# Performance work log

Measured on AMD Instinct MI355X. Metric: run time of the kernel, lower is better.

## Reference

```python
import jax, jax.numpy as jnp
import numpy as np


def setup_inputs() -> dict:
    key = jax.random.key(0)
    k1, k2, k3, k4 = jax.random.split(key, 4)
    B, C, H, W = 8, 512, 64, 64  # h must equal w per the broadcast in the original
    opt = jax.random.normal(k1, (B, C, H, W), dtype=jnp.float32)
    sar = jax.random.normal(k2, (B, C, H, W), dtype=jnp.float32)
    # 1x1 conv weights, shape [out_c, in_c] (kernel spatial dims are 1x1)
    W_opt = jax.random.normal(k3, (C, C), dtype=jnp.float32) * (2.0 / C) ** 0.5
    W_sar = jax.random.normal(k4, (C, C), dtype=jnp.float32) * (2.0 / C) ** 0.5
    return {"opt": opt, "sar": sar, "W_opt": W_opt, "W_sar": W_sar}


def _branch(x, Wc):
    # 1x1 conv: per-pixel channel mixing. Q = K = V (same conv applied to same input).
    f = jnp.einsum('oc,bchw->bohw', Wc, x)            # (b,c,h,w)
    # S[b,c,i,j] = sum_h Q[b,c,h,i] * K[b,c,h,j]  (transpose(2,3) @ original)
    S = jnp.einsum('bchi,bchj->bcij', f, f)           # (b,c,w,w)
    # nn.Softmax() with no dim on 4D -> softmax over channel dim (axis=1)
    S = jax.nn.softmax(S, axis=1)
    return f, S


def reference(opt, sar, W_opt, W_sar):
    V_opt, S_opt = _branch(opt, W_opt)
    V_sar, S_sar = _branch(sar, W_sar)
    hadamard = S_opt * S_sar                          # (b,c,w,w); h==w lets it broadcast with V
    Att = (V_opt * hadamard) * (V_sar * hadamard)
    return Att
```

## Files before the change

kernel.cpp:

```cpp
#include <hip/hip_runtime.h>
#include <cstdint>

#define CCH 512
#define HW  4096
#define WDIM 64
#define NBATCH 8
#define CHW ((size_t)CCH * HW)

typedef __attribute__((ext_vector_type(8))) short bf16x8;
typedef __attribute__((ext_vector_type(4))) float f32x4;

__device__ __forceinline__ unsigned short f2bf(float x) {
  unsigned u = __float_as_uint(x);
  unsigned r = (u + 0x7FFFu + ((u >> 16) & 1u)) >> 16;
  return (unsigned short)r;
}
__device__ __forceinline__ float bf2f(unsigned short h) {
  return __uint_as_float(((unsigned)h) << 16);
}

__device__ __forceinline__ void gl_lds16(const void* g, void* l) {
  __builtin_amdgcn_global_load_lds(
      (const __attribute__((address_space(1))) void*)g,
      (__attribute__((address_space(3))) void*)l, 16, 0, 0);
}

__global__ __launch_bounds__(256) void wsplit_k(
    const float* __restrict__ Wo, const float* __restrict__ Wsr,
    unsigned short* __restrict__ Whl) {
  const int br = blockIdx.y;
  const float* W = br ? Wsr : Wo;
  const int i = blockIdx.x * 256 + threadIdx.x;
  const float x = W[i];
  const unsigned short h = f2bf(x);
  unsigned short* dst = Whl + (size_t)br * 524288;
  dst[i] = h;
  dst[262144 + i] = f2bf(x - bf2f(h));
}

__global__ __launch_bounds__(256) void splitT_k(
    const float* __restrict__ opt, const float* __restrict__ sar,
    unsigned short* __restrict__ Xth, unsigned short* __restrict__ Xtl,
    int b0) {
  const int z = blockIdx.z;
  const int br = z & 1, bl = z >> 1;
  const float* X = (br ? sar : opt) + (size_t)(b0 + bl) * CHW;
  unsigned short* oh = Xth + (size_t)z * CHW;
  unsigned short* ol = Xtl + (size_t)z * CHW;
  const int p0 = blockIdx.x * 64, c0 = blockIdx.y * 64;

  __shared__ float ts[64][65];
  const int tid = threadIdx.x;

  const int pl = (tid & 15) * 4;
#pragma unroll
  for (int rr = 0; rr < 4; ++rr) {
    const int cl = rr * 16 + (tid >> 4);
    float4 v = *(const float4*)&X[(size_t)(c0 + cl) * HW + p0 + pl];
    ts[cl][pl + 0] = v.x;
    ts[cl][pl + 1] = v.y;
    ts[cl][pl + 2] = v.z;
    ts[cl][pl + 3] = v.w;
  }
  __syncthreads();

  const int prow = tid >> 2;
  const int cch = (tid & 3) * 16;
  unsigned short hb[16], lb[16];
#pragma unroll
  for (int k = 0; k < 16; ++k) {
    const float x = ts[cch + k][prow];
    const unsigned short h = f2bf(x);
    hb[k] = h;
    lb[k] = f2bf(x - bf2f(h));
  }
  const size_t ob = (size_t)(p0 + prow) * CCH + c0 + cch;
  *(uint4*)&oh[ob] = *(uint4*)&hb[0];
  *(uint4*)&oh[ob + 8] = *(uint4*)&hb[8];
  *(uint4*)&ol[ob] = *(uint4*)&lb[0];
  *(uint4*)&ol[ob + 8] = *(uint4*)&lb[8];
}

__global__ __launch_bounds__(256, 4) void mfma_conv_k(
    const unsigned short* __restrict__ Whl,
    const unsigned short* __restrict__ Xth,
    const unsigned short* __restrict__ Xtl,
    float* __restrict__ F) {
  const int z = blockIdx.z;
  const int br = z & 1;
  const unsigned short* Ah_g = Whl + (size_t)br * 524288;
  const unsigned short* Al_g = Ah_g + 262144;
  const unsigned short* Bh_g = Xth + (size_t)z * CHW;
  const unsigned short* Bl_g = Xtl + (size_t)z * CHW;
  const int n0 = blockIdx.x * 128, m0 = blockIdx.y * 128;

  __shared__ unsigned short Ahs[128 * 32];
  __shared__ unsigned short Als[128 * 32];
  __shared__ unsigned short Bhs[128 * 32];
  __shared__ unsigned short Bls[128 * 32];

  const int tid = threadIdx.x;
  const int wave = tid >> 6, lane = tid & 63;
  const int wm = (wave >> 1) * 64, wn = (wave & 1) * 64;

  f32x4 acc[4][4] = {};

  const int rl = lane >> 2;
  const int kc = (((lane & 3) ^ ((lane >> 3) & 3)) * 8);

  for (int k0 = 0; k0 < CCH; k0 += 32) {
    __syncthreads();
#pragma unroll
    for (int q = 0; q < 2; ++q) {
      const int rbase = wave * 32 + q * 16;
      const int r = rbase + rl;
      gl_lds16(Ah_g + (size_t)(m0 + r) * CCH + k0 + kc, &Ahs[rbase * 32]);
      gl_lds16(Al_g + (size_t)(m0 + r) * CCH + k0 + kc, &Als[rbase * 32]);
      gl_lds16(Bh_g + (size_t)(n0 + r) * CCH + k0 + kc, &Bhs[rbase * 32]);
      gl_lds16(Bl_g + (size_t)(n0 + r) * CCH + k0 + kc, &Bls[rbase * 32]);
    }
    __syncthreads();

    const int fr = lane & 15;
    const int kh = (((lane >> 4) ^ ((lane >> 1) & 3)) * 8);
    bf16x8 ah[4], al[4], bh[4], bl[4];
#pragma unroll
    for (int i = 0; i < 4; ++i) {
      ah[i] = *(const bf16x8*)&Ahs[(wm + i * 16 + fr) * 32 + kh];
      al[i] = *(const bf16x8*)&Als[(wm + i * 16 + fr) * 32 + kh];
      bh[i] = *(const bf16x8*)&Bhs[(wn + i * 16 + fr) * 32 + kh];
      bl[i] = *(const bf16x8*)&Bls[(wn + i * 16 + fr) * 32 + kh];
    }
#pragma unroll
    for (int i = 0; i < 4; ++i)
#pragma unroll
      for (int j = 0; j < 4; ++j) {
        acc[i][j] = __builtin_amdgcn_mfma_f32_16x16x32_bf16(ah[i], bh[j], acc[i][j], 0, 0, 0);
        acc[i][j] = __builtin_amdgcn_mfma_f32_16x16x32_bf16(ah[i], bl[j], acc[i][j], 0, 0, 0);
        acc[i][j] = __builtin_amdgcn_mfma_f32_16x16x32_bf16(al[i], bh[j], acc[i][j], 0, 0, 0);
      }
  }

  float* Fb = F + (size_t)z * CHW;
  const int col = lane & 15, rq = (lane >> 4) * 4;
#pragma unroll
  for (int i = 0; i < 4; ++i)
#pragma unroll
    for (int j = 0; j < 4; ++j) {
      const int n = n0 + wn + j * 16 + col;
#pragma unroll
      for (int r = 0; r < 4; ++r) {
        const int m = m0 + wm + i * 16 + rq + r;
        Fb[(size_t)m * HW + n] = acc[i][j][r];
      }
    }
}

#define FT_S 72
__global__ __launch_bounds__(256, 4) void gram_k(
    const float* __restrict__ F, float* __restrict__ S) {
  const size_t base = ((size_t)blockIdx.y * CCH + blockIdx.x) * HW;
  const float* Fc = F + base;
  float* Sc = S + base;

  __shared__ float Fs[64][68];
  __shared__ unsigned short FtH[64 * FT_S];
  __shared__ unsigned short FtL[64 * FT_S];

  const int tid = threadIdx.x;

  {
    const int h = tid >> 2;
    const int w0 = (tid & 3) * 16;
    const float* src = &Fc[h * 64 + w0];
    float4 v0 = *(const float4*)(src + 0);
    float4 v1 = *(const float4*)(src + 4);
    float4 v2 = *(const float4*)(src + 8);
    float4 v3 = *(const float4*)(src + 12);
    *(float4*)&Fs[h][w0 + 0]  = v0;
    *(float4*)&Fs[h][w0 + 4]  = v1;
    *(float4*)&Fs[h][w0 + 8]  = v2;
    *(float4*)&Fs[h][w0 + 12] = v3;
  }
  __syncthreads();

  {
    const int w = tid & 63;
    const int hc = (tid >> 6) * 16;
    unsigned short hb[16], lb[16];
#pragma unroll
    for (int k = 0; k < 16; ++k) {
      const float x = Fs[hc + k][w];
      const unsigned short h = f2bf(x);
      hb[k] = h;
      lb[k] = f2bf(x - bf2f(h));
    }
    unsigned short* dh = &FtH[w * FT_S + hc];
    unsigned short* dl = &FtL[w * FT_S + hc];
    *(uint4*)(dh + 0) = *(uint4*)&hb[0];
    *(uint4*)(dh + 8) = *(uint4*)&hb[8];
    *(uint4*)(dl + 0) = *(uint4*)&lb[0];
    *(uint4*)(dl + 8) = *(uint4*)&lb[8];
  }
  __syncthreads();

  const int wave = tid >> 6, lane = tid & 63;
  const int wm = (wave >> 1) * 32, wn = (wave & 1) * 32;
  const int fr = lane & 15, kq = (lane >> 4) * 8;

  f32x4 acc[2][2] = {};
#pragma unroll
  for (int kcc = 0; kcc < 2; ++kcc) {
    bf16x8 ah[2], al[2], bh[2], bl[2];
#pragma unroll
    for (int i = 0; i < 2; ++i) {
      ah[i] = *(const bf16x8*)&FtH[(wm + i * 16 + fr) * FT_S + kcc * 32 + kq];
      al[i] = *(const bf16x8*)&FtL[(wm + i * 16 + fr) * FT_S + kcc * 32 + kq];
      bh[i] = *(const bf16x8*)&FtH[(wn + i * 16 + fr) * FT_S + kcc * 32 + kq];
      bl[i] = *(const bf16x8*)&FtL[(wn + i * 16 + fr) * FT_S + kcc * 32 + kq];
    }
#pragma unroll
    for (int i = 0; i < 2; ++i)
#pragma unroll
      for (int j = 0; j < 2; ++j) {
        acc[i][j] = __builtin_amdgcn_mfma_f32_16x16x32_bf16(ah[i], bh[j], acc[i][j], 0, 0, 0);
        acc[i][j] = __builtin_amdgcn_mfma_f32_16x16x32_bf16(ah[i], bl[j], acc[i][j], 0, 0, 0);
        acc[i][j] = __builtin_amdgcn_mfma_f32_16x16x32_bf16(al[i], bh[j], acc[i][j], 0, 0, 0);
      }
  }

  const int rq = (lane >> 4) * 4;
#pragma unroll
  for (int i = 0; i < 2; ++i)
#pragma unroll
    for (int j = 0; j < 2; ++j) {
      const int n = wn + j * 16 + fr;
#pragma unroll
      for (int r = 0; r < 4; ++r) {
        const int m = wm + i * 16 + rq + r;
        Sc[m * 64 + n] = acc[i][j][r];
      }
    }
}

__global__ __launch_bounds__(1024, 8) void softmax_fuse_k(
    const float* __restrict__ S, const float* __restrict__ Fbuf,
    float* __restrict__ Out) {
  const int i = blockIdx.x;
  const int b = blockIdx.y;
  const int tid = threadIdx.x;
  const int jl = (tid & 15) * 4;
  const int g = tid >> 4;

  const size_t rowO = (size_t)(b * 2) * CHW + (size_t)i * WDIM;
  const size_t rowS = rowO + CHW;

  float mo[4], lo[4], ms[4], ls[4];
#pragma unroll
  for (int k = 0; k < 4; ++k) { mo[k] = -1e30f; lo[k] = 0.f; ms[k] = -1e30f; ls[k] = 0.f; }

#pragma unroll
  for (int cc = 0; cc < 8; ++cc) {
    const int c = g * 8 + cc;
    const size_t off = (size_t)c * HW + jl;
    float4 xo = *(const float4*)&S[rowO + off];
    float4 xs = *(const float4*)&S[rowS + off];
    float xov[4] = {xo.x, xo.y, xo.z, xo.w};
    float xsv[4] = {xs.x, xs.y, xs.z, xs.w};
#pragma unroll
    for (int k = 0; k < 4; ++k) {
      float nm = fmaxf(mo[k], xov[k]);
      lo[k] = lo[k] * __expf(mo[k] - nm) + __expf(xov[k] - nm);
      mo[k] = nm;
      nm = fmaxf(ms[k], xsv[k]);
      ls[k] = ls[k] * __expf(ms[k] - nm) + __expf(xsv[k] - nm);
      ms[k] = nm;
    }
  }

  __shared__ float sm[2][64][64];
  __shared__ float sl[2][64][64];
  __shared__ float Mf[2][64];
  __shared__ float Li[2][64];

  *(float4*)&sm[0][g][jl] = make_float4(mo[0], mo[1], mo[2], mo[3]);
  *(float4*)&sl[0][g][jl] = make_float4(lo[0], lo[1], lo[2], lo[3]);
  *(float4*)&sm[1][g][jl] = make_float4(ms[0], ms[1], ms[2], ms[3]);
  *(float4*)&sl[1][g][jl] = make_float4(ls[0], ls[1], ls[2], ls[3]);
  __syncthreads();

  if (tid < 128) {
    const int br = tid >> 6, j = tid & 63;
    float M = -1e30f;
#pragma unroll 16
    for (int t = 0; t < 64; ++t) M = fmaxf(M, sm[br][t][j]);
    float L = 0.f;
#pragma unroll 16
    for (int t = 0; t < 64; ++t) L += sl[br][t][j] * __expf(sm[br][t][j] - M);
    Mf[br][j] = M;
    Li[br][j] = 1.f / L;
  }
  __syncthreads();

  float4 Mo4 = *(const float4*)&Mf[0][jl];
  float4 iLo4 = *(const float4*)&Li[0][jl];
  float4 Ms4 = *(const float4*)&Mf[1][jl];
  float4 iLs4 = *(const float4*)&Li[1][jl];
  float Mov[4] = {Mo4.x, Mo4.y, Mo4.z, Mo4.w};
  float iLov[4] = {iLo4.x, iLo4.y, iLo4.z, iLo4.w};
  float Msv[4] = {Ms4.x, Ms4.y, Ms4.z, Ms4.w};
  float iLsv[4] = {iLs4.x, iLs4.y, iLs4.z, iLs4.w};

#pragma unroll
  for (int cc = 0; cc < 8; ++cc) {
    const int c = g * 8 + cc;
    const size_t off = (size_t)c * HW + jl;
    float4 xo = *(const float4*)&S[rowO + off];
    float4 xs = *(const float4*)&S[rowS + off];
    float4 fo = *(const float4*)&Fbuf[rowO + off];
    float4 fs = *(const float4*)&Fbuf[rowS + off];
    float xov[4] = {xo.x, xo.y, xo.z, xo.w};
    float xsv[4] = {xs.x, xs.y, xs.z, xs.w};
    float fov[4] = {fo.x, fo.y, fo.z, fo.w};
    float fsv[4] = {fs.x, fs.y, fs.z, fs.w};
    float ov[4];
#pragma unroll
    for (int k = 0; k < 4; ++k) {
      const float ho = __expf(xov[k] - Mov[k]) * iLov[k];
      const float hs = __expf(xsv[k] - Msv[k]) * iLsv[k];
      float h2 = ho * hs;
      h2 *= h2;
      ov[k] = fov[k] * fsv[k] * h2;
    }
    *(float4*)&Out[(size_t)b * CHW + (size_t)c * HW + (size_t)i * WDIM + jl] =
        make_float4(ov[0], ov[1], ov[2], ov[3]);
  }
}

extern "C" void kernel_launch(void* const* d_in, const int* in_sizes, int n_in,
                              void* d_out, int out_size, void* d_ws, size_t ws_size,
                              hipStream_t stream) {
  const float* opt = (const float*)d_in[0];
  const float* sar = (const float*)d_in[1];
  const float* Wo  = (const float*)d_in[2];
  const float* Wsr = (const float*)d_in[3];
  float* out = (float*)d_out;

  unsigned short* Whl = (unsigned short*)d_ws;
  const size_t whlElems = 2u * 2u * 262144u;
  const size_t perBl = 2 * CHW;
  const size_t perBlBytes = perBl * 8;
  int bc = (int)((ws_size - whlElems * 2) / perBlBytes);
  if (bc < 1) bc = 1;
  if (bc > NBATCH) bc = NBATCH;
  const int passes = (NBATCH + bc - 1) / bc;
  const int nbp = (NBATCH + passes - 1) / passes;

  unsigned short* Xth = Whl + whlElems;
  unsigned short* Xtl = Xth + (size_t)bc * perBl;
  float* Fbuf = (float*)(Xtl + (size_t)bc * perBl);
  float* Sbuf = (float*)Xth;

  hipLaunchKernelGGL(wsplit_k, dim3(1024, 2), dim3(256), 0, stream, Wo, Wsr, Whl);

  for (int b0 = 0; b0 < NBATCH; b0 += nbp) {
    const int nb = (NBATCH - b0 < nbp) ? (NBATCH - b0) : nbp;

    hipLaunchKernelGGL(splitT_k, dim3(64, 8, nb * 2), dim3(256), 0, stream,
                       opt, sar, Xth, Xtl, b0);

    hipLaunchKernelGGL(mfma_conv_k, dim3(32, 4, nb * 2), dim3(256), 0, stream,
                       Whl, Xth, Xtl, Fbuf);

    hipLaunchKernelGGL(gram_k, dim3(CCH, nb * 2), dim3(256), 0, stream,
                       Fbuf, Sbuf);

    hipLaunchKernelGGL(softmax_fuse_k, dim3(WDIM, nb), dim3(1024), 0, stream,
                       Sbuf, Fbuf, out + (size_t)b0 * CHW);
  }
}
```

Measured before the change: 419.5 us.

## Fuse input transpose and bf16 hi/lo split into the conv GEMM kernel

Removes the separate splitT_k pass that transposed the fp32 inputs into bf16 hi/lo buffers. The conv GEMM now loads fp32 input tiles directly into LDS with a rotated column layout and splits them into hi/lo bf16 in registers before the MFMAs. This drops a full write and reread of the intermediate buffers and one launch per pass. In exchange it doubles LDS traffic for the B operand, adds per-iteration conversion ALU work, and changes the split to truncation instead of round-to-nearest.

```diff
diff --git a/kernel.cpp b/kernel.cpp
--- a/kernel.cpp
+++ b/kernel.cpp
@@ -38,66 +38,20 @@
   dst[262144 + i] = f2bf(x - bf2f(h));
 }
 
-__global__ __launch_bounds__(256) void splitT_k(
+__global__ __launch_bounds__(256, 4) void mfma_conv_k(
+    const unsigned short* __restrict__ Whl,
     const float* __restrict__ opt, const float* __restrict__ sar,
-    unsigned short* __restrict__ Xth, unsigned short* __restrict__ Xtl,
-    int b0) {
+    float* __restrict__ F, int b0) {
   const int z = blockIdx.z;
   const int br = z & 1, bl = z >> 1;
-  const float* X = (br ? sar : opt) + (size_t)(b0 + bl) * CHW;
-  unsigned short* oh = Xth + (size_t)z * CHW;
-  unsigned short* ol = Xtl + (size_t)z * CHW;
-  const int p0 = blockIdx.x * 64, c0 = blockIdx.y * 64;
-
-  __shared__ float ts[64][65];
-  const int tid = threadIdx.x;
-
-  const int pl = (tid & 15) * 4;
-#pragma unroll
-  for (int rr = 0; rr < 4; ++rr) {
-    const int cl = rr * 16 + (tid >> 4);
-    float4 v = *(const float4*)&X[(size_t)(c0 + cl) * HW + p0 + pl];
-    ts[cl][pl + 0] = v.x;
-    ts[cl][pl + 1] = v.y;
-    ts[cl][pl + 2] = v.z;
-    ts[cl][pl + 3] = v.w;
-  }
-  __syncthreads();
-
-  const int prow = tid >> 2;
-  const int cch = (tid & 3) * 16;
-  unsigned short hb[16], lb[16];
-#pragma unroll
-  for (int k = 0; k < 16; ++k) {
-    const float x = ts[cch + k][prow];
-    const unsigned short h = f2bf(x);
-    hb[k] = h;
-    lb[k] = f2bf(x - bf2f(h));
-  }
-  const size_t ob = (size_t)(p0 + prow) * CCH + c0 + cch;
-  *(uint4*)&oh[ob] = *(uint4*)&hb[0];
-  *(uint4*)&oh[ob + 8] = *(uint4*)&hb[8];
-  *(uint4*)&ol[ob] = *(uint4*)&lb[0];
-  *(uint4*)&ol[ob + 8] = *(uint4*)&lb[8];
-}
-
-__global__ __launch_bounds__(256, 4) void mfma_conv_k(
-    const unsigned short* __restrict__ Whl,
-    const unsigned short* __restrict__ Xth,
-    const unsigned short* __restrict__ Xtl,
-    float* __restrict__ F) {
-  const int z = blockIdx.z;
-  const int br = z & 1;
   const unsigned short* Ah_g = Whl + (size_t)br * 524288;
   const unsigned short* Al_g = Ah_g + 262144;
-  const unsigned short* Bh_g = Xth + (size_t)z * CHW;
-  const unsigned short* Bl_g = Xtl + (size_t)z * CHW;
+  const float* Xb = (br ? sar : opt) + (size_t)(b0 + bl) * CHW;
   const int n0 = blockIdx.x * 128, m0 = blockIdx.y * 128;
 
   __shared__ unsigned short Ahs[128 * 32];
   __shared__ unsigned short Als[128 * 32];
-  __shared__ unsigned short Bhs[128 * 32];
-  __shared__ unsigned short Bls[128 * 32];
+  __shared__ float Xs[32 * 128];
 
   const int tid = threadIdx.x;
   const int wave = tid >> 6, lane = tid & 63;
@@ -106,7 +60,14 @@
   f32x4 acc[4][4] = {};
 
   const int rl = lane >> 2;
-  const int kc = (((lane & 3) ^ ((lane >> 3) & 3)) * 8);
+  const int kcA = (((lane & 3) ^ ((lane >> 3) & 3)) * 8);
+
+  const int brow_off = wave * 2 + (lane >> 5);
+  const int bcol = (lane & 31) * 4;
+
+  const int fr = lane & 15;
+  const int quad = lane >> 4;
+  const int khA = ((quad ^ ((lane >> 1) & 3)) * 8);
 
   for (int k0 = 0; k0 < CCH; k0 += 32) {
     __syncthreads();
@@ -114,31 +75,47 @@
     for (int q = 0; q < 2; ++q) {
       const int rbase = wave * 32 + q * 16;
       const int r = rbase + rl;
-      gl_lds16(Ah_g + (size_t)(m0 + r) * CCH + k0 + kc, &Ahs[rbase * 32]);
-      gl_lds16(Al_g + (size_t)(m0 + r) * CCH + k0 + kc, &Als[rbase * 32]);
-      gl_lds16(Bh_g + (size_t)(n0 + r) * CCH + k0 + kc, &Bhs[rbase * 32]);
-      gl_lds16(Bl_g + (size_t)(n0 + r) * CCH + k0 + kc, &Bls[rbase * 32]);
+      gl_lds16(Ah_g + (size_t)(m0 + r) * CCH + k0 + kcA, &Ahs[rbase * 32]);
+      gl_lds16(Al_g + (size_t)(m0 + r) * CCH + k0 + kcA, &Als[rbase * 32]);
+    }
+#pragma unroll
+    for (int t = 0; t < 4; ++t) {
+      const int row = t * 8 + brow_off;
+      const int srccol = (bcol + 128 - 8 * t) & 127;
+      gl_lds16(&Xb[(size_t)(k0 + row) * HW + n0 + srccol],
+               &Xs[t * 1024 + wave * 256]);
     }
     __syncthreads();
 
-    const int fr = lane & 15;
-    const int kh = (((lane >> 4) ^ ((lane >> 1) & 3)) * 8);
-    bf16x8 ah[4], al[4], bh[4], bl[4];
+    bf16x8 ah[4], al[4];
 #pragma unroll
     for (int i = 0; i < 4; ++i) {
-      ah[i] = *(const bf16x8*)&Ahs[(wm + i * 16 + fr) * 32 + kh];
-      al[i] = *(const bf16x8*)&Als[(wm + i * 16 + fr) * 32 + kh];
-      bh[i] = *(const bf16x8*)&Bhs[(wn + i * 16 + fr) * 32 + kh];
-      bl[i] = *(const bf16x8*)&Bls[(wn + i * 16 + fr) * 32 + kh];
-    }
-#pragma unroll
-    for (int i = 0; i < 4; ++i)
-#pragma unroll
-      for (int j = 0; j < 4; ++j) {
-        acc[i][j] = __builtin_amdgcn_mfma_f32_16x16x32_bf16(ah[i], bh[j], acc[i][j], 0, 0, 0);
-        acc[i][j] = __builtin_amdgcn_mfma_f32_16x16x32_bf16(ah[i], bl[j], acc[i][j], 0, 0, 0);
-        acc[i][j] = __builtin_amdgcn_mfma_f32_16x16x32_bf16(al[i], bh[j], acc[i][j], 0, 0, 0);
-      }
+      ah[i] = *(const bf16x8*)&Ahs[(wm + i * 16 + fr) * 32 + khA];
+      al[i] = *(const bf16x8*)&Als[(wm + i * 16 + fr) * 32 + khA];
+    }
+
+#pragma unroll
+    for (int j = 0; j < 4; ++j) {
+      const int colj = (wn + j * 16 + fr + 8 * quad) & 127;
+      unsigned short hs[8], ls[8];
+#pragma unroll
+      for (int s = 0; s < 8; ++s) {
+        const float x = Xs[(quad * 8 + s) * 128 + colj];
+        const unsigned xu = __float_as_uint(x);
+        const float hi = __uint_as_float(xu & 0xFFFF0000u);
+        const float lof = x - hi;
+        hs[s] = (unsigned short)(xu >> 16);
+        ls[s] = (unsigned short)(__float_as_uint(lof) >> 16);
+      }
+      const bf16x8 bh = *(const bf16x8*)hs;
+      const bf16x8 bl = *(const bf16x8*)ls;
+#pragma unroll
+      for (int i = 0; i < 4; ++i) {
+        acc[i][j] = __builtin_amdgcn_mfma_f32_16x16x32_bf16(ah[i], bh, acc[i][j], 0, 0, 0);
+        acc[i][j] = __builtin_amdgcn_mfma_f32_16x16x32_bf16(ah[i], bl, acc[i][j], 0, 0, 0);
+        acc[i][j] = __builtin_amdgcn_mfma_f32_16x16x32_bf16(al[i], bh, acc[i][j], 0, 0, 0);
+      }
+    }
   }
 
   float* Fb = F + (size_t)z * CHW;
@@ -356,21 +333,16 @@
   const int passes = (NBATCH + bc - 1) / bc;
   const int nbp = (NBATCH + passes - 1) / passes;
 
-  unsigned short* Xth = Whl + whlElems;
-  unsigned short* Xtl = Xth + (size_t)bc * perBl;
-  float* Fbuf = (float*)(Xtl + (size_t)bc * perBl);
-  float* Sbuf = (float*)Xth;
+  float* Fbuf = (float*)(Whl + whlElems);
+  float* Sbuf = Fbuf + (size_t)bc * perBl;
 
   hipLaunchKernelGGL(wsplit_k, dim3(1024, 2), dim3(256), 0, stream, Wo, Wsr, Whl);
 
   for (int b0 = 0; b0 < NBATCH; b0 += nbp) {
     const int nb = (NBATCH - b0 < nbp) ? (NBATCH - b0) : nbp;
 
-    hipLaunchKernelGGL(splitT_k, dim3(64, 8, nb * 2), dim3(256), 0, stream,
-                       opt, sar, Xth, Xtl, b0);
-
     hipLaunchKernelGGL(mfma_conv_k, dim3(32, 4, nb * 2), dim3(256), 0, stream,
-                       Whl, Xth, Xtl, Fbuf);
+                       Whl, opt, sar, Fbuf, b0);
 
     hipLaunchKernelGGL(gram_k, dim3(CCH, nb * 2), dim3(256), 0, stream,
                        Fbuf, Sbuf);
```

Measured after the change: 395.2 us. 1.06x faster.
